# Kernel optimization log

Measured on AMD Instinct MI355X. Metric: run time of the kernel, lower is better.

Reference implementation:

```python
import jax, jax.numpy as jnp
import numpy as np
import math

NUM_CELLS = 256
INPUT_DIM = 512
N_TOKENS = 131072
INIT_TEMP = 0.95


def setup_inputs() -> dict:
    key = jax.random.key(0)
    k_x, k_p, k_g = jax.random.split(key, 3)
    x = jax.random.normal(k_x, (N_TOKENS, INPUT_DIM), dtype=jnp.float32)
    prototypes = jax.random.normal(k_p, (NUM_CELLS, INPUT_DIM), dtype=jnp.float32)
    grid_pos = jax.random.normal(k_g, (NUM_CELLS, INPUT_DIM), dtype=jnp.float32)
    temp_raw = jnp.array([math.log(INIT_TEMP / (1.0 - INIT_TEMP))], dtype=jnp.float32)
    gate_logits = jnp.zeros((NUM_CELLS,), dtype=jnp.float32)
    return {"x": x, "prototypes": prototypes, "grid_pos": grid_pos,
            "temp_raw": temp_raw, "gate_logits": gate_logits}


def _cdist(x, y):
    # x: [N, D], y: [C, D] -> euclidean distances [N, C]
    d2 = (jnp.sum(x * x, axis=-1, keepdims=True)
          + jnp.sum(y * y, axis=-1)[None, :]
          - 2.0 * (x @ y.T))
    return jnp.sqrt(jnp.maximum(d2, 0.0))


def reference(x, prototypes, grid_pos, temp_raw, gate_logits):
    # temperature = sigmoid(temp_raw) * (1 - 0.001) + 0.001  (scalar)
    temperature = jax.nn.sigmoid(temp_raw[0]) * (1.0 - 0.001) + 0.001
    gate = jax.nn.sigmoid(gate_logits)[None, :]            # [1, C]
    d_total = _cdist(x, prototypes) + _cdist(x, grid_pos)  # [N, C]
    weights = jax.nn.softmax(-d_total / temperature, axis=-1) * gate
    weights = weights / (jnp.sum(weights, axis=-1, keepdims=True) + 1e-8)
    blended = weights @ prototypes                          # [N, D]
    # match torch shapes: blended [N,1,D], weights [N,1,C]
    return blended[:, None, :], weights[:, None, :]
```

## Files before the change

### kernel.cpp

```cpp
#include <hip/hip_runtime.h>
#include <hip/hip_bf16.h>

#define NCELLS 256
#define DIM    512
#define NTOK   131072

typedef __attribute__((ext_vector_type(8))) short  bf16x8;
typedef __attribute__((ext_vector_type(4))) float  f32x4;
typedef __attribute__((ext_vector_type(4))) short  s16x4;

static __device__ __forceinline__ unsigned short f2bf(float f) {
    union { float f; unsigned u; } v; v.f = f;
    unsigned r = v.u + 0x7fffu + ((v.u >> 16) & 1u);
    return (unsigned short)(r >> 16);
}
static __device__ __forceinline__ float bf2f(unsigned short h) {
    union { unsigned u; float f; } v; v.u = ((unsigned)h) << 16;
    return v.f;
}
static __device__ __forceinline__ bf16x8 cvt8(f32x4 a, f32x4 b) {
    bf16x8 r;
    r[0] = (short)f2bf(a[0]); r[1] = (short)f2bf(a[1]);
    r[2] = (short)f2bf(a[2]); r[3] = (short)f2bf(a[3]);
    r[4] = (short)f2bf(b[0]); r[5] = (short)f2bf(b[1]);
    r[6] = (short)f2bf(b[2]); r[7] = (short)f2bf(b[3]);
    return r;
}

static __device__ __forceinline__ void stage8k(const unsigned short* __restrict__ gsrc,
                                               unsigned short* l, int tid) {
    __builtin_amdgcn_global_load_lds(
        (const __attribute__((address_space(1))) unsigned int*)(gsrc + tid * 8),
        (__attribute__((address_space(3))) unsigned int*)(l + tid * 8),
        16, 0, 0);
}

__global__ void __launch_bounds__(256) prep_kernel(
        const float* __restrict__ proto, const float* __restrict__ grid,
        const float* __restrict__ temp_raw, const float* __restrict__ gate_logits,
        unsigned short* __restrict__ pcombL,
        unsigned short* __restrict__ protoTL,
        float* __restrict__ pp, float* __restrict__ gg,
        float* __restrict__ gate, float* __restrict__ invT)
{
    const int c = blockIdx.x;
    const int t = threadIdx.x;
    const int rl = c & 15, ct = c >> 4;
    float sp = 0.f, sg = 0.f;
    for (int i = t; i < DIM; i += 256) {
        float pv = proto[c * DIM + i];
        float gv = grid[c * DIM + i];
        const int h = i >> 8, kb2 = (i & 255) >> 3, e = i & 7;
        const int roff = rl * 256 + ((kb2 ^ (rl & 7)) << 3) + e;
        pcombL[(ct * 4 + h) * 4096 + roff]     = f2bf(pv);
        pcombL[(ct * 4 + 2 + h) * 4096 + roff] = f2bf(gv);
        const int d2 = i >> 4, rowd = i & 15;
        protoTL[d2 * 4096 + rowd * 256 + (((c >> 3) ^ (i & 7)) << 3) + (c & 7)] = f2bf(pv);
        sp += pv * pv; sg += gv * gv;
    }
    for (int m = 1; m < 64; m <<= 1) { sp += __shfl_xor(sp, m); sg += __shfl_xor(sg, m); }
    __shared__ float redp[4], redg[4];
    const int wv = t >> 6;
    if ((t & 63) == 0) { redp[wv] = sp; redg[wv] = sg; }
    __syncthreads();
    if (t == 0) {
        pp[c] = redp[0] + redp[1] + redp[2] + redp[3];
        gg[c] = redg[0] + redg[1] + redg[2] + redg[3];
        gate[c] = 1.f / (1.f + expf(-gate_logits[c]));
        if (c == 0) {
            float T = (1.f / (1.f + expf(-temp_raw[0]))) * (1.f - 0.001f) + 0.001f;
            invT[0] = 1.f / T;
        }
    }
}

#define WAIT_BAR(N) do { \
    asm volatile("s_waitcnt vmcnt(" #N ")" ::: "memory"); \
    __builtin_amdgcn_s_barrier(); \
    asm volatile("" ::: "memory"); \
} while (0)

__global__ void __launch_bounds__(512, 2) som_main(
        const float* __restrict__ x,
        const unsigned short* __restrict__ pcombL,
        const unsigned short* __restrict__ protoTL,
        const float* __restrict__ pp, const float* __restrict__ gg,
        const float* __restrict__ gate, const float* __restrict__ invTp,
        float* __restrict__ out_blend, float* __restrict__ out_w)
{
    const int tid  = threadIdx.x;
    const int lane = tid & 63;
    const int wv   = tid >> 6;
    const int tb   = blockIdx.x * 128 + wv * 16;
    const int r    = lane & 15;
    const int g    = lane >> 4;
    const int k8   = g * 8;

    __shared__ __align__(16) unsigned short sbuf[2][4096];
    __shared__ __align__(16) unsigned short lds_w[8][16][256];

    const float invT = invTp[0];

    stage8k(pcombL, sbuf[0], tid);

    bf16x8 a1[16];
    float xx_part = 0.f;
    const float* xrow = x + (size_t)(tb + r) * DIM;
    #pragma unroll
    for (int ks = 0; ks < 16; ++ks) {
        const f32x4* p0 = (const f32x4*)(xrow + ks * 32 + k8);
        f32x4 u0 = p0[0], u1 = p0[1];
        #pragma unroll
        for (int i = 0; i < 4; ++i) xx_part += u0[i] * u0[i] + u1[i] * u1[i];
        a1[ks] = cvt8(u0, u1);
    }
    xx_part += __shfl_xor(xx_part, 16);
    xx_part += __shfl_xor(xx_part, 32);
    float xt[4];
    #pragma unroll
    for (int j = 0; j < 4; ++j) xt[j] = __shfl(xx_part, g * 4 + j);

    #define CHUNK(ACC, HB, CH) do { \
        WAIT_BAR(0); \
        stage8k(((CH) < 63 ? pcombL + ((CH) + 1) * 4096 : protoTL), sbuf[((CH) + 1) & 1], tid); \
        const unsigned short* bb = sbuf[(CH) & 1]; \
        _Pragma("unroll") \
        for (int ks = 0; ks < 8; ++ks) { \
            bf16x8 b = *(const bf16x8*)(bb + r * 256 + (((ks * 4 + g) ^ (r & 7)) << 3)); \
            ACC = __builtin_amdgcn_mfma_f32_16x16x32_bf16(a1[(HB) * 8 + ks], b, ACC, 0, 0, 0); \
        } \
    } while (0)

    float s1[4] = {0.f, 0.f, 0.f, 0.f};
    float s2[4] = {0.f, 0.f, 0.f, 0.f};
    #pragma unroll 1
    for (int ctl = 0; ctl < 16; ++ctl) {
        f32x4 accP = {0.f, 0.f, 0.f, 0.f};
        f32x4 accG = {0.f, 0.f, 0.f, 0.f};
        CHUNK(accP, 0, ctl * 4 + 0);
        CHUNK(accP, 1, ctl * 4 + 1);
        CHUNK(accG, 0, ctl * 4 + 2);
        CHUNK(accG, 1, ctl * 4 + 3);
        const int cell = ctl * 16 + r;
        const float ppc = pp[cell], ggc = gg[cell], gtc = gate[cell];
        #pragma unroll
        for (int j = 0; j < 4; ++j) {
            float dp = sqrtf(fmaxf(xt[j] + ppc - 2.f * accP[j], 0.f));
            float dg = sqrtf(fmaxf(xt[j] + ggc - 2.f * accG[j], 0.f));
            float zj = 64.f - (dp + dg) * invT;
            float ep = __expf(zj);
            float eg = ep * gtc;
            s1[j] += ep;
            s2[j] += eg;
            const int tok = g * 4 + j;
            lds_w[wv][tok][(((ctl * 2 + (r >> 3)) ^ (tok & 7)) << 3) + (r & 7)] = f2bf(eg);
        }
    }
    #undef CHUNK

    float rden[4];
    #pragma unroll
    for (int j = 0; j < 4; ++j) {
        float a = s1[j], b = s2[j];
        a += __shfl_xor(a, 1); b += __shfl_xor(b, 1);
        a += __shfl_xor(a, 2); b += __shfl_xor(b, 2);
        a += __shfl_xor(a, 4); b += __shfl_xor(b, 4);
        a += __shfl_xor(a, 8); b += __shfl_xor(b, 8);
        rden[j] = 1.f / (b + 1e-8f * a);
    }

    float* wout = out_w + (size_t)tb * NCELLS;
    #pragma unroll
    for (int t0 = 0; t0 < 16; ++t0) {
        float rdt = __shfl(rden[t0 & 3], (t0 >> 2) * 16);
        const int addr = (((lane >> 1) ^ (t0 & 7)) << 3) + (lane & 1) * 4;
        s16x4 q = *(const s16x4*)&lds_w[wv][t0][addr];
        f32x4 o;
        o[0] = bf2f((unsigned short)q[0]) * rdt;
        o[1] = bf2f((unsigned short)q[1]) * rdt;
        o[2] = bf2f((unsigned short)q[2]) * rdt;
        o[3] = bf2f((unsigned short)q[3]) * rdt;
        *(f32x4*)&wout[(size_t)t0 * NCELLS + lane * 4] = o;
    }

    bf16x8 aw[8];
    #pragma unroll
    for (int ks = 0; ks < 8; ++ks)
        aw[ks] = *(const bf16x8*)&lds_w[wv][r][((ks * 4 + g) ^ (r & 7)) << 3];

    float* bout = out_blend + (size_t)tb * DIM;
    #pragma unroll 1
    for (int d2 = 0; d2 < 32; ++d2) {
        WAIT_BAR(4);
        if (d2 < 31) stage8k(protoTL + (d2 + 1) * 4096, sbuf[(d2 + 1) & 1], tid);
        const unsigned short* bb = sbuf[d2 & 1];
        f32x4 acc = {0.f, 0.f, 0.f, 0.f};
        #pragma unroll
        for (int ks = 0; ks < 8; ++ks) {
            bf16x8 b = *(const bf16x8*)(bb + r * 256 + (((ks * 4 + g) ^ (r & 7)) << 3));
            acc = __builtin_amdgcn_mfma_f32_16x16x32_bf16(aw[ks], b, acc, 0, 0, 0);
        }
        #pragma unroll
        for (int j = 0; j < 4; ++j)
            bout[(size_t)(g * 4 + j) * DIM + d2 * 16 + r] = acc[j] * rden[j];
    }
}

extern "C" void kernel_launch(void* const* d_in, const int* in_sizes, int n_in,
                              void* d_out, int out_size, void* d_ws, size_t ws_size,
                              hipStream_t stream) {
    const float* x           = (const float*)d_in[0];
    const float* proto       = (const float*)d_in[1];
    const float* grid        = (const float*)d_in[2];
    const float* temp_raw    = (const float*)d_in[3];
    const float* gate_logits = (const float*)d_in[4];

    float* out       = (float*)d_out;
    float* out_blend = out;
    float* out_w     = out + (size_t)NTOK * DIM;

    char* ws = (char*)d_ws;
    unsigned short* pcombL  = (unsigned short*)(ws);
    unsigned short* protoTL = (unsigned short*)(ws + 524288);
    float* pp   = (float*)(ws + 786432);
    float* gg   = (float*)(ws + 787456);
    float* gate = (float*)(ws + 788480);
    float* invT = (float*)(ws + 789504);

    prep_kernel<<<dim3(NCELLS), dim3(256), 0, stream>>>(
        proto, grid, temp_raw, gate_logits, pcombL, protoTL, pp, gg, gate, invT);
    som_main<<<dim3(NTOK / 128), dim3(512), 0, stream>>>(
        x, pcombL, protoTL, pp, gg, gate, invT, out_blend, out_w);
}
```

Before: 355.5 us.

## Load MFMA B operands directly from global in fragment order, drop LDS staging

Removes the barrier-synchronized double-buffered LDS staging of prototype/grid tiles. The prep kernel now writes B operands in per-lane MFMA fragment order so each lane reads its bf16x8 straight from global/L2. Blocks shrink from 512 to 256 threads with 64 tokens each, which removes block-wide barriers and allows more independent blocks per CU. The cost is that every wave fetches its B data separately from cache instead of sharing one LDS copy per block, which raises L2 traffic.

New measurement: 431.8 us. 21.5% more time.

```diff
diff --git a/kernel.cpp b/kernel.cpp
--- a/kernel.cpp
+++ b/kernel.cpp
@@ -27,35 +27,29 @@
     return r;
 }
 
-static __device__ __forceinline__ void stage8k(const unsigned short* __restrict__ gsrc,
-                                               unsigned short* l, int tid) {
-    __builtin_amdgcn_global_load_lds(
-        (const __attribute__((address_space(1))) unsigned int*)(gsrc + tid * 8),
-        (__attribute__((address_space(3))) unsigned int*)(l + tid * 8),
-        16, 0, 0);
-}
-
 __global__ void __launch_bounds__(256) prep_kernel(
         const float* __restrict__ proto, const float* __restrict__ grid,
         const float* __restrict__ temp_raw, const float* __restrict__ gate_logits,
-        unsigned short* __restrict__ pcombL,
-        unsigned short* __restrict__ protoTL,
+        unsigned short* __restrict__ pcombB,
+        unsigned short* __restrict__ protoB,
         float* __restrict__ pp, float* __restrict__ gg,
         float* __restrict__ gate, float* __restrict__ invT)
 {
     const int c = blockIdx.x;
     const int t = threadIdx.x;
-    const int rl = c & 15, ct = c >> 4;
+    const int ct = c >> 4, rl = c & 15;
+    const int cs = c >> 5, cg = (c >> 3) & 3, ce = c & 7;
     float sp = 0.f, sg = 0.f;
     for (int i = t; i < DIM; i += 256) {
         float pv = proto[c * DIM + i];
         float gv = grid[c * DIM + i];
-        const int h = i >> 8, kb2 = (i & 255) >> 3, e = i & 7;
-        const int roff = rl * 256 + ((kb2 ^ (rl & 7)) << 3) + e;
-        pcombL[(ct * 4 + h) * 4096 + roff]     = f2bf(pv);
-        pcombL[(ct * 4 + 2 + h) * 4096 + roff] = f2bf(gv);
-        const int d2 = i >> 4, rowd = i & 15;
-        protoTL[d2 * 4096 + rowd * 256 + (((c >> 3) ^ (i & 7)) << 3) + (c & 7)] = f2bf(pv);
+        const int s = i >> 5, gq = (i >> 3) & 3, e = i & 7;
+        const size_t uP = ((size_t)((ct * 2 + 0) * 16 + s) * 64 + gq * 16 + rl) * 8 + e;
+        const size_t uG = ((size_t)((ct * 2 + 1) * 16 + s) * 64 + gq * 16 + rl) * 8 + e;
+        pcombB[uP] = f2bf(pv);
+        pcombB[uG] = f2bf(gv);
+        const int dt = i >> 4, rr = i & 15;
+        protoB[((size_t)(dt * 8 + cs) * 64 + cg * 16 + rr) * 8 + ce] = f2bf(pv);
         sp += pv * pv; sg += gv * gv;
     }
     for (int m = 1; m < 64; m <<= 1) { sp += __shfl_xor(sp, m); sg += __shfl_xor(sg, m); }
@@ -74,16 +68,10 @@
     }
 }
 
-#define WAIT_BAR(N) do { \
-    asm volatile("s_waitcnt vmcnt(" #N ")" ::: "memory"); \
-    __builtin_amdgcn_s_barrier(); \
-    asm volatile("" ::: "memory"); \
-} while (0)
-
-__global__ void __launch_bounds__(512, 2) som_main(
+__global__ void __launch_bounds__(256) som_main(
         const float* __restrict__ x,
-        const unsigned short* __restrict__ pcombL,
-        const unsigned short* __restrict__ protoTL,
+        const unsigned short* __restrict__ pcombB,
+        const unsigned short* __restrict__ protoB,
         const float* __restrict__ pp, const float* __restrict__ gg,
         const float* __restrict__ gate, const float* __restrict__ invTp,
         float* __restrict__ out_blend, float* __restrict__ out_w)
@@ -91,17 +79,14 @@
     const int tid  = threadIdx.x;
     const int lane = tid & 63;
     const int wv   = tid >> 6;
-    const int tb   = blockIdx.x * 128 + wv * 16;
+    const int tb   = blockIdx.x * 64 + wv * 16;
     const int r    = lane & 15;
     const int g    = lane >> 4;
     const int k8   = g * 8;
 
-    __shared__ __align__(16) unsigned short sbuf[2][4096];
-    __shared__ __align__(16) unsigned short lds_w[8][16][256];
+    __shared__ __align__(16) unsigned short lds_w[4][16][256];
 
     const float invT = invTp[0];
-
-    stage8k(pcombL, sbuf[0], tid);
 
     bf16x8 a1[16];
     float xx_part = 0.f;
@@ -120,28 +105,21 @@
     #pragma unroll
     for (int j = 0; j < 4; ++j) xt[j] = __shfl(xx_part, g * 4 + j);
 
-    #define CHUNK(ACC, HB, CH) do { \
-        WAIT_BAR(0); \
-        stage8k(((CH) < 63 ? pcombL + ((CH) + 1) * 4096 : protoTL), sbuf[((CH) + 1) & 1], tid); \
-        const unsigned short* bb = sbuf[(CH) & 1]; \
-        _Pragma("unroll") \
-        for (int ks = 0; ks < 8; ++ks) { \
-            bf16x8 b = *(const bf16x8*)(bb + r * 256 + (((ks * 4 + g) ^ (r & 7)) << 3)); \
-            ACC = __builtin_amdgcn_mfma_f32_16x16x32_bf16(a1[(HB) * 8 + ks], b, ACC, 0, 0, 0); \
-        } \
-    } while (0)
-
     float s1[4] = {0.f, 0.f, 0.f, 0.f};
     float s2[4] = {0.f, 0.f, 0.f, 0.f};
+    const int lo = g * 16 + r;
     #pragma unroll 1
-    for (int ctl = 0; ctl < 16; ++ctl) {
+    for (int ct = 0; ct < 16; ++ct) {
+        const bf16x8* bP = (const bf16x8*)pcombB + (size_t)(ct * 2) * 16 * 64 + lo;
+        const bf16x8* bG = bP + 16 * 64;
         f32x4 accP = {0.f, 0.f, 0.f, 0.f};
         f32x4 accG = {0.f, 0.f, 0.f, 0.f};
-        CHUNK(accP, 0, ctl * 4 + 0);
-        CHUNK(accP, 1, ctl * 4 + 1);
-        CHUNK(accG, 0, ctl * 4 + 2);
-        CHUNK(accG, 1, ctl * 4 + 3);
-        const int cell = ctl * 16 + r;
+        #pragma unroll
+        for (int s = 0; s < 16; ++s) {
+            accP = __builtin_amdgcn_mfma_f32_16x16x32_bf16(a1[s], bP[s * 64], accP, 0, 0, 0);
+            accG = __builtin_amdgcn_mfma_f32_16x16x32_bf16(a1[s], bG[s * 64], accG, 0, 0, 0);
+        }
+        const int cell = ct * 16 + r;
         const float ppc = pp[cell], ggc = gg[cell], gtc = gate[cell];
         #pragma unroll
         for (int j = 0; j < 4; ++j) {
@@ -153,10 +131,9 @@
             s1[j] += ep;
             s2[j] += eg;
             const int tok = g * 4 + j;
-            lds_w[wv][tok][(((ctl * 2 + (r >> 3)) ^ (tok & 7)) << 3) + (r & 7)] = f2bf(eg);
+            lds_w[wv][tok][(((ct * 2 + (r >> 3)) ^ (tok & 7)) << 3) + (r & 7)] = f2bf(eg);
         }
     }
-    #undef CHUNK
 
     float rden[4];
     #pragma unroll
@@ -190,19 +167,15 @@
 
     float* bout = out_blend + (size_t)tb * DIM;
     #pragma unroll 1
-    for (int d2 = 0; d2 < 32; ++d2) {
-        WAIT_BAR(4);
-        if (d2 < 31) stage8k(protoTL + (d2 + 1) * 4096, sbuf[(d2 + 1) & 1], tid);
-        const unsigned short* bb = sbuf[d2 & 1];
+    for (int dt = 0; dt < 32; ++dt) {
+        const bf16x8* bT = (const bf16x8*)protoB + (size_t)dt * 8 * 64 + lo;
         f32x4 acc = {0.f, 0.f, 0.f, 0.f};
         #pragma unroll
-        for (int ks = 0; ks < 8; ++ks) {
-            bf16x8 b = *(const bf16x8*)(bb + r * 256 + (((ks * 4 + g) ^ (r & 7)) << 3));
-            acc = __builtin_amdgcn_mfma_f32_16x16x32_bf16(aw[ks], b, acc, 0, 0, 0);
-        }
+        for (int s = 0; s < 8; ++s)
+            acc = __builtin_amdgcn_mfma_f32_16x16x32_bf16(aw[s], bT[s * 64], acc, 0, 0, 0);
         #pragma unroll
         for (int j = 0; j < 4; ++j)
-            bout[(size_t)(g * 4 + j) * DIM + d2 * 16 + r] = acc[j] * rden[j];
+            bout[(size_t)(g * 4 + j) * DIM + dt * 16 + r] = acc[j] * rden[j];
     }
 }
 
@@ -220,15 +193,15 @@
     float* out_w     = out + (size_t)NTOK * DIM;
 
     char* ws = (char*)d_ws;
-    unsigned short* pcombL  = (unsigned short*)(ws);
-    unsigned short* protoTL = (unsigned short*)(ws + 524288);
+    unsigned short* pcombB = (unsigned short*)(ws);
+    unsigned short* protoB = (unsigned short*)(ws + 524288);
     float* pp   = (float*)(ws + 786432);
     float* gg   = (float*)(ws + 787456);
     float* gate = (float*)(ws + 788480);
     float* invT = (float*)(ws + 789504);
 
     prep_kernel<<<dim3(NCELLS), dim3(256), 0, stream>>>(
-        proto, grid, temp_raw, gate_logits, pcombL, protoTL, pp, gg, gate, invT);
-    som_main<<<dim3(NTOK / 128), dim3(512), 0, stream>>>(
-        x, pcombL, protoTL, pp, gg, gate, invT, out_blend, out_w);
-}
+        proto, grid, temp_raw, gate_logits, pcombB, protoB, pp, gg, gate, invT);
+    som_main<<<dim3(NTOK / 64), dim3(256), 0, stream>>>(
+        x, pcombB, protoB, pp, gg, gate, invT, out_blend, out_w);
+}
```
